# Kernel optimization log

Measured on AMD Instinct MI355X. Metric: run time of the kernel, lower is better.

## Reference

```python
import jax, jax.numpy as jnp
import numpy as np

GRID = 28
P = GRID * GRID  # 784 grid points
BY = 1.0 / 13.5  # grid spacing from DTMWeightWrapperLayer(by=1/13.5)
_c = BY * np.stack(np.meshgrid(np.arange(GRID), np.arange(GRID), indexing='ij'), -1).reshape(P, 2).astype(np.float32)
_D2np = ((_c[:, None, :] - _c[None, :, :]) ** 2).sum(-1)
_ORDERnp = np.argsort(_D2np, axis=1)  # per-grid-point neighbor order (constant)
D2S = jnp.asarray(np.take_along_axis(_D2np, _ORDERnp, axis=1), dtype=jnp.float32)  # [P,P] sorted sq dists
ORDER = jnp.asarray(_ORDERnp, dtype=jnp.int32)
TSEQ_A = jnp.asarray(np.linspace(0.06, 0.3, 25), dtype=jnp.float32); KK_A = (0, 1)
TSEQ_B = jnp.asarray(np.linspace(0.14, 0.4, 27), dtype=jnp.float32); KK_B = (0, 1, 2)

def _conv(x, k):
    return jax.lax.conv_general_dilated(x, k, (1, 1), 'SAME', dimension_numbers=('NHWC', 'HWIO', 'NHWC'))

def _dtm(w, m0):
    # distance-to-measure: w [B,P] nonneg weights on the 28x28 grid -> dtm values [B,P]
    ws = w[:, ORDER]                      # [B,P,P] weights ordered by distance from each grid point
    cum = jnp.cumsum(ws, axis=-1)
    m0W = m0 * jnp.sum(w, axis=-1)[:, None, None]  # mass threshold per sample
    eff = jnp.clip(m0W - (cum - ws), 0.0, ws)      # effective weight used from each neighbor
    return jnp.sqrt(jnp.sum(eff * D2S[None], axis=-1) / m0W[:, :, 0])

def _topo(f, tseq, kk, W, b):
    # persistence-landscape features: lambda_k(t) = k-th largest tent value over grid points
    tmax = tseq[-1]
    tent = jnp.maximum(0.0, jnp.minimum(tseq[None, :, None] - f[:, None, :], (tmax - tseq)[None, :, None]))  # [B,T,P]
    top, _ = jax.lax.top_k(tent, max(kk) + 1)       # [B,T,kmax]
    lam = top[..., jnp.asarray(kk)]                 # [B,T,|KK|]
    return lam.reshape(f.shape[0], -1) @ W + b

def setup_inputs() -> dict:
    key = jax.random.key(0)
    ks = jax.random.split(key, 16)
    r = lambda i, s: (0.05 * jax.random.normal(ks[i], s)).astype(jnp.float32)
    z = lambda n: jnp.zeros((n,), jnp.float32)
    return {
        'x': jax.random.uniform(ks[0], (16, 28, 28, 1), jnp.float32),
        'k11': r(1, (3, 3, 1, 32)), 'cb11': z(32), 'k12': r(2, (3, 3, 32, 1)), 'cb12': z(1),
        'k31': r(3, (3, 3, 1, 32)), 'cb31': z(32), 'k32': r(4, (3, 3, 32, 1)), 'cb32': z(1),
        'k41': r(5, (3, 3, 1, 32)), 'cb41': z(32), 'k42': r(6, (3, 3, 32, 1)), 'cb42': z(1),
        'W33': r(7, (50, 16)), 'b33': z(16), 'W43': r(8, (81, 16)), 'b43': z(16),
        'W5': r(9, (50, 16)), 'b5': z(16), 'W6': r(10, (81, 16)), 'b6': z(16),
        'W7': r(11, (848, 64)), 'b7': z(64), 'W8': r(12, (64, 10)), 'b8': z(10),
    }

def reference(x, k11, cb11, k12, cb12, k31, cb31, k32, cb32, k41, cb41, k42, cb42,
              W33, b33, W43, b43, W5, b5, W6, b6, W7, b7, W8, b8):
    relu = jax.nn.relu
    B = 16
    # CNN branch on raw image
    x1 = relu(_conv(relu(_conv(x, k11) + cb11), k12) + cb12).reshape(B, P)
    # DTM functions on the grid
    x2 = x.reshape(B, P)
    x2_1 = _dtm(x2, 0.05)
    x2_2 = _dtm(x2, 0.2)
    # CNN on DTM(m0=0.05) then topo layer
    x3 = relu(_conv(relu(_conv(x2_1.reshape(B, GRID, GRID, 1), k31) + cb31), k32) + cb32).reshape(B, P)
    x3 = relu(_topo(x3, TSEQ_A, KK_A, W33, b33))
    # CNN on DTM(m0=0.2) then topo layer
    x4 = relu(_conv(relu(_conv(x2_2.reshape(B, GRID, GRID, 1), k41) + cb41), k42) + cb42).reshape(B, P)
    x4 = relu(_topo(x4, TSEQ_B, KK_B, W43, b43))
    # topo layers directly on DTM functions
    x5 = relu(_topo(x2_1, TSEQ_A, KK_A, W5, b5))
    x6 = relu(_topo(x2_2, TSEQ_B, KK_B, W6, b6))
    xc = jnp.concatenate((x1, x3, x4, x5, x6), axis=-1)  # [16,848]
    return relu(xc @ W7 + b7) @ W8 + b8  # [16,10]
```

## Files before the change

kernel.cpp:

```cpp
#include <hip/hip_runtime.h>
#include <math.h>

#define GRID 28
#define NP 784
#define PADW 82
#define PADOFF 27

struct PairTab { unsigned int pk[NP]; float d2[NP]; };
constexpr PairTab make_pairs() {
    PairTab t{};
    int cnt[1459] = {};
    for (int di = 0; di < GRID; ++di)
        for (int dj = 0; dj < GRID; ++dj) cnt[di*di + dj*dj]++;
    int off[1459] = {};
    int acc = 0;
    for (int s = 0; s < 1459; ++s) { off[s] = acc; acc += cnt[s]; }
    const double BY2 = (1.0/13.5) * (1.0/13.5);
    for (int di = 0; di < GRID; ++di)
        for (int dj = 0; dj < GRID; ++dj) {
            int s = di*di + dj*dj;
            int o = off[s]++;
            t.pk[o] = (unsigned)(((di*PADW) << 6) | dj);
            t.d2[o] = (float)((double)s * BY2);
        }
    return t;
}
__constant__ PairTab d_PT = make_pairs();

__global__ __launch_bounds__(1024) void dtm_kernel(const float* __restrict__ x,
        float* __restrict__ ws)
{
    __shared__ float wpad[PADW*PADW];
    __shared__ float red[16];
    float* out1 = ws;
    float* out2 = ws + 12544;

    const int blk = blockIdx.x;
    const int img = blk / 49, grp = blk % 49;
    const int tid = threadIdx.x;
    const int w = tid >> 6, lane = tid & 63;

    for (int i = tid; i < PADW*PADW; i += 1024) wpad[i] = 0.f;
    float v = 0.f;
    if (tid < NP) v = x[img*NP + tid];
    __syncthreads();
    if (tid < NP) wpad[(tid/GRID + PADOFF)*PADW + (tid % GRID) + PADOFF] = v;
    for (int off = 32; off; off >>= 1) v += __shfl_down(v, off, 64);
    if (lane == 0) red[w] = v;
    __syncthreads();
    float sumw = 0.f;
    #pragma unroll
    for (int i = 0; i < 16; ++i) sumw += red[i];

    const int pix  = grp*16 + w;
    const int base = (pix/GRID + PADOFF)*PADW + (pix % GRID) + PADOFF;
    const float m0W1 = 0.05f * sumw;
    const float m0W2 = 0.2f  * sumw;
    float a1 = 0.f, a2 = 0.f, carry = 0.f;

    for (int k0 = 0; k0 < NP; k0 += 64) {
        const int idx = k0 + lane;
        const int ii  = idx < NP ? idx : NP-1;
        const unsigned p = d_PT.pk[ii];
        const float dd   = d_PT.d2[ii];
        const int a  = (int)(p >> 6);
        const int bb = (int)(p & 63u);
        const float w00 = wpad[base + a + bb];
        const float w01 = wpad[base + a - bb];
        const float w10 = wpad[base - a + bb];
        const float w11 = wpad[base - a - bb];
        float Wg = w00;
        Wg += (bb ? w01 : 0.f);
        Wg += (a  ? w10 : 0.f);
        Wg += ((a && bb) ? w11 : 0.f);
        if (idx >= NP) Wg = 0.f;
        float incl = Wg;
        #pragma unroll
        for (int d = 1; d < 64; d <<= 1) {
            const float t = __shfl_up(incl, d, 64);
            if (lane >= d) incl += t;
        }
        const float cumb = carry + (incl - Wg);
        const float e1 = fminf(fmaxf(m0W1 - cumb, 0.f), Wg);
        const float e2 = fminf(fmaxf(m0W2 - cumb, 0.f), Wg);
        a1 = fmaf(e1, dd, a1);
        a2 = fmaf(e2, dd, a2);
        carry += __shfl(incl, 63, 64);
        if (carry >= m0W2) break;
    }
    for (int m = 32; m; m >>= 1) { a1 += __shfl_xor(a1, m, 64); a2 += __shfl_xor(a2, m, 64); }
    if (lane == 0) {
        out1[img*NP + pix] = sqrtf(a1 / m0W1);
        out2[img*NP + pix] = sqrtf(a2 / m0W2);
    }
}

__device__ void conv_path_g(const float* __restrict__ inRow,
                            const float* __restrict__ kA, const float* __restrict__ cbA,
                            const float* __restrict__ kB, const float* __restrict__ cbB,
                            float* __restrict__ outRow, int r0, float* smem)
{
    float* inl = smem;
    float* kAl = inl + 308;
    float* cbl = kAl + 288;
    float* kBl = cbl + 32;
    float* h   = kBl + 288;
    const int tid = threadIdx.x;
    const float cbB0 = cbB[0];

    for (int i = tid; i < 288; i += 1024) { kAl[i] = kA[i]; kBl[i] = kB[i]; }
    if (tid < 32) cbl[tid] = cbA[tid];
    for (int i = tid; i < 11*GRID; i += 1024) {
        const int lr = i / GRID, xx = i % GRID;
        const int y = r0 - 2 + lr;
        inl[i] = (y >= 0 && y < GRID) ? inRow[y*GRID + xx] : 0.f;
    }
    __syncthreads();

    for (int o = tid; o < 9*GRID*32; o += 1024) {
        const int c = o & 31;
        const int pos = o >> 5;
        const int xx = pos % GRID;
        const int lr = pos / GRID;
        const int y = r0 - 1 + lr;
        if ((unsigned)y < GRID) {
            float a = cbl[c];
            #pragma unroll
            for (int dy = 0; dy < 3; ++dy) {
                const int iy = y + dy - 1;
                if ((unsigned)iy >= GRID) continue;
                const int il = iy - (r0 - 2);
                #pragma unroll
                for (int dx = 0; dx < 3; ++dx) {
                    const int ix = xx + dx - 1;
                    if ((unsigned)ix < GRID)
                        a = fmaf(inl[il*GRID + ix], kAl[(dy*3 + dx)*32 + c], a);
                }
            }
            h[(lr*GRID + xx)*33 + c] = fmaxf(a, 0.f);
        }
    }
    __syncthreads();

    if (tid < 4*7*GRID) {
        const int o = tid >> 2, part = tid & 3;
        const int xx = o % GRID, ly = o / GRID;
        const int y = r0 + ly;
        float a = 0.f;
        #pragma unroll
        for (int dy = 0; dy < 3; ++dy) {
            const int yy = y + dy - 1;
            if ((unsigned)yy >= GRID) continue;
            const int lr = yy - (r0 - 1);
            #pragma unroll
            for (int dx = 0; dx < 3; ++dx) {
                const int x2 = xx + dx - 1;
                if ((unsigned)x2 >= GRID) continue;
                const float* hb = &h[(lr*GRID + x2)*33 + part*8];
                const float* kb = &kBl[(dy*3 + dx)*32 + part*8];
                #pragma unroll
                for (int c = 0; c < 8; ++c) a += hb[c] * kb[c];
            }
        }
        a += __shfl_xor(a, 1, 64);
        a += __shfl_xor(a, 2, 64);
        if (part == 0) outRow[y*GRID + xx] = fmaxf(a + cbB0, 0.f);
    }
}

__global__ __launch_bounds__(1024) void conv_kernel(const float* __restrict__ x,
        const float* __restrict__ k11, const float* __restrict__ cb11,
        const float* __restrict__ k12, const float* __restrict__ cb12,
        const float* __restrict__ k31, const float* __restrict__ cb31,
        const float* __restrict__ k32, const float* __restrict__ cb32,
        const float* __restrict__ k41, const float* __restrict__ cb41,
        const float* __restrict__ k42, const float* __restrict__ cb42,
        float* __restrict__ ws)
{
    __shared__ float smem[9232];
    const int blk = blockIdx.x;
    const float* x2_1 = ws;
    const float* x2_2 = ws + 12544;
    float* x1o = ws + 25088;
    float* x3c = ws + 37632;
    float* x4c = ws + 50176;

    if (blk < 64) {
        const int b = blk >> 2, q = blk & 3;
        conv_path_g(x + b*NP, k11, cb11, k12, cb12, x1o + b*NP, q*7, smem);
    } else if (blk < 128) {
        const int cidx = blk - 64;
        const int b = cidx >> 2, q = cidx & 3;
        conv_path_g(x2_1 + b*NP, k31, cb31, k32, cb32, x3c + b*NP, q*7, smem);
    } else {
        const int cidx = blk - 128;
        const int b = cidx >> 2, q = cidx & 3;
        conv_path_g(x2_2 + b*NP, k41, cb41, k42, cb42, x4c + b*NP, q*7, smem);
    }
}

__device__ __forceinline__ float tseqA(int i) {
    if (i == 24) return 0.3f;
    return (float)((double)i * ((0.3 - 0.06)/24.0) + 0.06);
}
__device__ __forceinline__ float tseqB(int i) {
    if (i == 26) return 0.4f;
    return (float)((double)i * ((0.4 - 0.14)/26.0) + 0.14);
}

__device__ __forceinline__ void merge3(float& m0, float& m1, float& m2,
                                       float b0, float b1, float b2) {
    float r0, r1, r2;
    if (m0 <= b0) {
        r0 = m0;
        if (m1 <= b0) { r1 = m1; r2 = fminf(m2, b0); }
        else          { r1 = b0; r2 = fminf(m1, b1); }
    } else {
        r0 = b0;
        if (b1 <= m0) { r1 = b1; r2 = fminf(b2, m0); }
        else          { r1 = m0; r2 = fminf(m1, b1); }
    }
    m0 = r0; m1 = r1; m2 = r2;
}

__global__ __launch_bounds__(1024) void tail_kernel(
        const float* __restrict__ W33, const float* __restrict__ b33,
        const float* __restrict__ W43, const float* __restrict__ b43,
        const float* __restrict__ W5,  const float* __restrict__ b5,
        const float* __restrict__ W6,  const float* __restrict__ b6,
        const float* __restrict__ W7,  const float* __restrict__ b7,
        const float* __restrict__ W8,  const float* __restrict__ b8,
        const float* __restrict__ ws,  float* __restrict__ out)
{
    __shared__ float xc[848];
    __shared__ float part[1024];
    __shared__ float h7[64];
    __shared__ float fsh[16];
    const int b = blockIdx.x, tid = threadIdx.x;
    const int w = tid >> 6, lane = tid & 63;
    const float* x2_1 = ws;
    const float* x2_2 = ws + 12544;
    const float* x1o  = ws + 25088;
    const float* x3c  = ws + 37632;
    const float* x4c  = ws + 50176;

    if (tid < NP) xc[tid] = x1o[b*NP + tid];

    if (w < 4) {
        const float* src = (w == 0) ? x3c : (w == 1) ? x4c : (w == 2) ? x2_1 : x2_2;
        src += b*NP;
        float m0 = INFINITY, m1 = INFINITY, m2 = INFINITY;
        for (int i = lane; i < NP; i += 64) {
            const float v = src[i];
            if (v < m0)      { m2 = m1; m1 = m0; m0 = v; }
            else if (v < m1) { m2 = m1; m1 = v; }
            else if (v < m2) { m2 = v; }
        }
        for (int mask = 1; mask <= 32; mask <<= 1) {
            const float b0 = __shfl_xor(m0, mask, 64);
            const float b1 = __shfl_xor(m1, mask, 64);
            const float b2 = __shfl_xor(m2, mask, 64);
            merge3(m0, m1, m2, b0, b1, b2);
        }
        if (lane == 0) { fsh[w*3+0] = m0; fsh[w*3+1] = m1; fsh[w*3+2] = m2; }
    }
    __syncthreads();

    if (w < 4) {
        const int g = lane >> 4, j = lane & 15;
        const float f0 = fsh[w*3+0], f1 = fsh[w*3+1], f2 = fsh[w*3+2];
        float acc = 0.f;
        if (w == 0 || w == 2) {
            const float* Wm = (w == 0) ? W33 : W5;
            for (int i = g; i < 50; i += 4) {
                const int t = i >> 1, k = i & 1;
                const float ts = tseqA(t);
                const float fk = k ? f1 : f0;
                const float lam = fmaxf(fminf(ts - fk, 0.3f - ts), 0.f);
                acc = fmaf(lam, Wm[i*16 + j], acc);
            }
        } else {
            const float* Wm = (w == 1) ? W43 : W6;
            for (int i = g; i < 81; i += 4) {
                const int t = i / 3, k = i - t*3;
                const float ts = tseqB(t);
                const float fk = (k == 0) ? f0 : (k == 1 ? f1 : f2);
                const float lam = fmaxf(fminf(ts - fk, 0.4f - ts), 0.f);
                acc = fmaf(lam, Wm[i*16 + j], acc);
            }
        }
        acc += __shfl_xor(acc, 16, 64);
        acc += __shfl_xor(acc, 32, 64);
        if (lane < 16) {
            const float* bv = (w == 0) ? b33 : (w == 1) ? b43 : (w == 2) ? b5 : b6;
            xc[784 + w*16 + lane] = fmaxf(acc + bv[lane], 0.f);
        }
    }
    __syncthreads();

    {
        float acc = 0.f;
        const int i0 = w * 53;
        for (int i = i0; i < i0 + 53; ++i) acc = fmaf(xc[i], W7[i*64 + lane], acc);
        part[w*64 + lane] = acc;
    }
    __syncthreads();
    if (tid < 64) {
        float s = b7[tid];
        #pragma unroll
        for (int k = 0; k < 16; ++k) s += part[k*64 + tid];
        h7[tid] = fmaxf(s, 0.f);
    }
    __syncthreads();

    if (w < 10) {
        float a2 = h7[lane] * W8[lane*10 + w];
        for (int m = 32; m; m >>= 1) a2 += __shfl_down(a2, m, 64);
        if (lane == 0) out[b*10 + w] = a2 + b8[w];
    }
}

extern "C" void kernel_launch(void* const* d_in, const int* in_sizes, int n_in,
                              void* d_out, int out_size, void* d_ws, size_t ws_size,
                              hipStream_t stream)
{
    const float* x    = (const float*)d_in[0];
    const float* k11  = (const float*)d_in[1];
    const float* cb11 = (const float*)d_in[2];
    const float* k12  = (const float*)d_in[3];
    const float* cb12 = (const float*)d_in[4];
    const float* k31  = (const float*)d_in[5];
    const float* cb31 = (const float*)d_in[6];
    const float* k32  = (const float*)d_in[7];
    const float* cb32 = (const float*)d_in[8];
    const float* k41  = (const float*)d_in[9];
    const float* cb41 = (const float*)d_in[10];
    const float* k42  = (const float*)d_in[11];
    const float* cb42 = (const float*)d_in[12];
    const float* W33  = (const float*)d_in[13];
    const float* b33  = (const float*)d_in[14];
    const float* W43  = (const float*)d_in[15];
    const float* b43  = (const float*)d_in[16];
    const float* W5   = (const float*)d_in[17];
    const float* b5   = (const float*)d_in[18];
    const float* W6   = (const float*)d_in[19];
    const float* b6   = (const float*)d_in[20];
    const float* W7   = (const float*)d_in[21];
    const float* b7   = (const float*)d_in[22];
    const float* W8   = (const float*)d_in[23];
    const float* b8   = (const float*)d_in[24];
    float* ws  = (float*)d_ws;
    float* out = (float*)d_out;

    dtm_kernel <<<dim3(784), dim3(1024), 0, stream>>>(x, ws);
    conv_kernel<<<dim3(192), dim3(1024), 0, stream>>>(x, k11, cb11, k12, cb12,
                                                      k31, cb31, k32, cb32,
                                                      k41, cb41, k42, cb42, ws);
    tail_kernel<<<dim3(16),  dim3(1024), 0, stream>>>(W33, b33, W43, b43, W5, b5, W6, b6,
                                                      W7, b7, W8, b8, ws, out);
}
```

Measured before the change: 35.43 us.

## Fuse conv and tail kernels via last-block atomic counter; drop padded DTM smem

Merges the conv and tail kernels into one launch. Each image's 12 conv blocks bump a per-image atomic counter, and the last block to arrive runs the topo/MLP tail for that image. The counter is zeroed by block 0 of the preceding DTM kernel. Separately, the DTM kernel replaces the 82x82 zero-padded shared buffer with an unpadded 784-float image plus explicit bounds checks, which removes the zero-fill and a barrier. The cost is extra branch and predicate work in the DTM inner loop and a reliance on atomics plus fences for correctness.

```diff
diff --git a/kernel.cpp b/kernel.cpp
--- a/kernel.cpp
+++ b/kernel.cpp
@@ -3,8 +3,6 @@
 
 #define GRID 28
 #define NP 784
-#define PADW 82
-#define PADOFF 27
 
 struct PairTab { unsigned int pk[NP]; float d2[NP]; };
 constexpr PairTab make_pairs() {
@@ -20,7 +18,7 @@
         for (int dj = 0; dj < GRID; ++dj) {
             int s = di*di + dj*dj;
             int o = off[s]++;
-            t.pk[o] = (unsigned)(((di*PADW) << 6) | dj);
+            t.pk[o] = (unsigned)((di << 8) | dj);
             t.d2[o] = (float)((double)s * BY2);
         }
     return t;
@@ -30,7 +28,7 @@
 __global__ __launch_bounds__(1024) void dtm_kernel(const float* __restrict__ x,
         float* __restrict__ ws)
 {
-    __shared__ float wpad[PADW*PADW];
+    __shared__ float wimg[NP];
     __shared__ float red[16];
     float* out1 = ws;
     float* out2 = ws + 12544;
@@ -40,11 +38,10 @@
     const int tid = threadIdx.x;
     const int w = tid >> 6, lane = tid & 63;
 
-    for (int i = tid; i < PADW*PADW; i += 1024) wpad[i] = 0.f;
+    if (blk == 0 && tid < 16) ((int*)(ws + 62720))[tid] = 0;
+
     float v = 0.f;
-    if (tid < NP) v = x[img*NP + tid];
-    __syncthreads();
-    if (tid < NP) wpad[(tid/GRID + PADOFF)*PADW + (tid % GRID) + PADOFF] = v;
+    if (tid < NP) { v = x[img*NP + tid]; wimg[tid] = v; }
     for (int off = 32; off; off >>= 1) v += __shfl_down(v, off, 64);
     if (lane == 0) red[w] = v;
     __syncthreads();
@@ -52,8 +49,8 @@
     #pragma unroll
     for (int i = 0; i < 16; ++i) sumw += red[i];
 
-    const int pix  = grp*16 + w;
-    const int base = (pix/GRID + PADOFF)*PADW + (pix % GRID) + PADOFF;
+    const int pix = grp*16 + w;
+    const int pr = pix / GRID, pc = pix % GRID;
     const float m0W1 = 0.05f * sumw;
     const float m0W2 = 0.2f  * sumw;
     float a1 = 0.f, a2 = 0.f, carry = 0.f;
@@ -63,16 +60,18 @@
         const int ii  = idx < NP ? idx : NP-1;
         const unsigned p = d_PT.pk[ii];
         const float dd   = d_PT.d2[ii];
-        const int a  = (int)(p >> 6);
-        const int bb = (int)(p & 63u);
-        const float w00 = wpad[base + a + bb];
-        const float w01 = wpad[base + a - bb];
-        const float w10 = wpad[base - a + bb];
-        const float w11 = wpad[base - a - bb];
-        float Wg = w00;
-        Wg += (bb ? w01 : 0.f);
-        Wg += (a  ? w10 : 0.f);
-        Wg += ((a && bb) ? w11 : 0.f);
+        const int di = (int)(p >> 8);
+        const int dj = (int)(p & 255u);
+        const int dG = di * GRID;
+        const bool rpOK = (pr + di) < GRID;
+        const bool rmOK = pr >= di;
+        const bool cpOK = (pc + dj) < GRID;
+        const bool cmOK = pc >= dj;
+        float Wg = 0.f;
+        if (rpOK && cpOK)               Wg += wimg[pix + dG + dj];
+        if (dj && rpOK && cmOK)         Wg += wimg[pix + dG - dj];
+        if (di && rmOK && cpOK)         Wg += wimg[pix - dG + dj];
+        if (di && dj && rmOK && cmOK)   Wg += wimg[pix - dG - dj];
         if (idx >= NP) Wg = 0.f;
         float incl = Wg;
         #pragma unroll
@@ -168,37 +167,6 @@
     }
 }
 
-__global__ __launch_bounds__(1024) void conv_kernel(const float* __restrict__ x,
-        const float* __restrict__ k11, const float* __restrict__ cb11,
-        const float* __restrict__ k12, const float* __restrict__ cb12,
-        const float* __restrict__ k31, const float* __restrict__ cb31,
-        const float* __restrict__ k32, const float* __restrict__ cb32,
-        const float* __restrict__ k41, const float* __restrict__ cb41,
-        const float* __restrict__ k42, const float* __restrict__ cb42,
-        float* __restrict__ ws)
-{
-    __shared__ float smem[9232];
-    const int blk = blockIdx.x;
-    const float* x2_1 = ws;
-    const float* x2_2 = ws + 12544;
-    float* x1o = ws + 25088;
-    float* x3c = ws + 37632;
-    float* x4c = ws + 50176;
-
-    if (blk < 64) {
-        const int b = blk >> 2, q = blk & 3;
-        conv_path_g(x + b*NP, k11, cb11, k12, cb12, x1o + b*NP, q*7, smem);
-    } else if (blk < 128) {
-        const int cidx = blk - 64;
-        const int b = cidx >> 2, q = cidx & 3;
-        conv_path_g(x2_1 + b*NP, k31, cb31, k32, cb32, x3c + b*NP, q*7, smem);
-    } else {
-        const int cidx = blk - 128;
-        const int b = cidx >> 2, q = cidx & 3;
-        conv_path_g(x2_2 + b*NP, k41, cb41, k42, cb42, x4c + b*NP, q*7, smem);
-    }
-}
-
 __device__ __forceinline__ float tseqA(int i) {
     if (i == 24) return 0.3f;
     return (float)((double)i * ((0.3 - 0.06)/24.0) + 0.06);
@@ -223,26 +191,58 @@
     m0 = r0; m1 = r1; m2 = r2;
 }
 
-__global__ __launch_bounds__(1024) void tail_kernel(
+__global__ __launch_bounds__(1024) void conv_tail_kernel(const float* __restrict__ x,
+        const float* __restrict__ k11, const float* __restrict__ cb11,
+        const float* __restrict__ k12, const float* __restrict__ cb12,
+        const float* __restrict__ k31, const float* __restrict__ cb31,
+        const float* __restrict__ k32, const float* __restrict__ cb32,
+        const float* __restrict__ k41, const float* __restrict__ cb41,
+        const float* __restrict__ k42, const float* __restrict__ cb42,
         const float* __restrict__ W33, const float* __restrict__ b33,
         const float* __restrict__ W43, const float* __restrict__ b43,
         const float* __restrict__ W5,  const float* __restrict__ b5,
         const float* __restrict__ W6,  const float* __restrict__ b6,
         const float* __restrict__ W7,  const float* __restrict__ b7,
         const float* __restrict__ W8,  const float* __restrict__ b8,
-        const float* __restrict__ ws,  float* __restrict__ out)
+        float* __restrict__ ws, float* __restrict__ out)
 {
-    __shared__ float xc[848];
-    __shared__ float part[1024];
-    __shared__ float h7[64];
-    __shared__ float fsh[16];
-    const int b = blockIdx.x, tid = threadIdx.x;
-    const int w = tid >> 6, lane = tid & 63;
+    __shared__ float smem[9232];
+    __shared__ int lastFlag;
+    const int blk = blockIdx.x;
+    const int tid = threadIdx.x;
     const float* x2_1 = ws;
     const float* x2_2 = ws + 12544;
-    const float* x1o  = ws + 25088;
-    const float* x3c  = ws + 37632;
-    const float* x4c  = ws + 50176;
+    float* x1o = ws + 25088;
+    float* x3c = ws + 37632;
+    float* x4c = ws + 50176;
+    int* cnt = (int*)(ws + 62720);
+
+    int b;
+    if (blk < 64) {
+        b = blk >> 2;
+        conv_path_g(x + b*NP, k11, cb11, k12, cb12, x1o + b*NP, (blk & 3)*7, smem);
+    } else if (blk < 128) {
+        const int c = blk - 64; b = c >> 2;
+        conv_path_g(x2_1 + b*NP, k31, cb31, k32, cb32, x3c + b*NP, (c & 3)*7, smem);
+    } else {
+        const int c = blk - 128; b = c >> 2;
+        conv_path_g(x2_2 + b*NP, k41, cb41, k42, cb42, x4c + b*NP, (c & 3)*7, smem);
+    }
+
+    __threadfence();
+    __syncthreads();
+    if (tid == 0)
+        lastFlag = (__hip_atomic_fetch_add(&cnt[b], 1, __ATOMIC_ACQ_REL,
+                                           __HIP_MEMORY_SCOPE_AGENT) == 11);
+    __syncthreads();
+    if (!lastFlag) return;
+    __threadfence();
+
+    float* xc   = smem;
+    float* part = smem + 848;
+    float* h7   = smem + 1872;
+    float* fsh  = smem + 1936;
+    const int w = tid >> 6, lane = tid & 63;
 
     if (tid < NP) xc[tid] = x1o[b*NP + tid];
 
@@ -352,10 +352,11 @@
     float* ws  = (float*)d_ws;
     float* out = (float*)d_out;
 
-    dtm_kernel <<<dim3(784), dim3(1024), 0, stream>>>(x, ws);
-    conv_kernel<<<dim3(192), dim3(1024), 0, stream>>>(x, k11, cb11, k12, cb12,
-                                                      k31, cb31, k32, cb32,
-                                                      k41, cb41, k42, cb42, ws);
-    tail_kernel<<<dim3(16),  dim3(1024), 0, stream>>>(W33, b33, W43, b43, W5, b5, W6, b6,
-                                                      W7, b7, W8, b8, ws, out);
-}
+    dtm_kernel      <<<dim3(784), dim3(1024), 0, stream>>>(x, ws);
+    conv_tail_kernel<<<dim3(192), dim3(1024), 0, stream>>>(x, k11, cb11, k12, cb12,
+                                                           k31, cb31, k32, cb32,
+                                                           k41, cb41, k42, cb42,
+                                                           W33, b33, W43, b43, W5, b5,
+                                                           W6, b6, W7, b7, W8, b8,
+                                                           ws, out);
+}
```

After: 96.61 us. +172.7%, slower.

## Move raw-image conv into DTM launch and split convs into smaller row bands

Applied to the files above, without the earlier changes.

The raw-image CNN branch, which does not depend on the DTM, now runs inside the first launch alongside the DTM blocks, leaving the second launch with only the two DTM-dependent conv paths. Convolutions are split into 7 bands of 4 rows instead of 4 bands of 7, so the grid has more and smaller blocks with less halo recompute per block. The DTM no longer builds a zero-padded 82x82 shared image; it reads the unpadded 28x28 image with explicit bounds checks, which drops the clear loop and one barrier. The price is extra branch logic in the inner neighbor loop and less shared memory per block.

```diff
diff --git a/kernel.cpp b/kernel.cpp
--- a/kernel.cpp
+++ b/kernel.cpp
@@ -3,8 +3,6 @@
 
 #define GRID 28
 #define NP 784
-#define PADW 82
-#define PADOFF 27
 
 struct PairTab { unsigned int pk[NP]; float d2[NP]; };
 constexpr PairTab make_pairs() {
@@ -20,104 +18,37 @@
         for (int dj = 0; dj < GRID; ++dj) {
             int s = di*di + dj*dj;
             int o = off[s]++;
-            t.pk[o] = (unsigned)(((di*PADW) << 6) | dj);
+            t.pk[o] = (unsigned)((di << 8) | dj);
             t.d2[o] = (float)((double)s * BY2);
         }
     return t;
 }
 __constant__ PairTab d_PT = make_pairs();
 
-__global__ __launch_bounds__(1024) void dtm_kernel(const float* __restrict__ x,
-        float* __restrict__ ws)
-{
-    __shared__ float wpad[PADW*PADW];
-    __shared__ float red[16];
-    float* out1 = ws;
-    float* out2 = ws + 12544;
-
-    const int blk = blockIdx.x;
-    const int img = blk / 49, grp = blk % 49;
-    const int tid = threadIdx.x;
-    const int w = tid >> 6, lane = tid & 63;
-
-    for (int i = tid; i < PADW*PADW; i += 1024) wpad[i] = 0.f;
-    float v = 0.f;
-    if (tid < NP) v = x[img*NP + tid];
-    __syncthreads();
-    if (tid < NP) wpad[(tid/GRID + PADOFF)*PADW + (tid % GRID) + PADOFF] = v;
-    for (int off = 32; off; off >>= 1) v += __shfl_down(v, off, 64);
-    if (lane == 0) red[w] = v;
-    __syncthreads();
-    float sumw = 0.f;
-    #pragma unroll
-    for (int i = 0; i < 16; ++i) sumw += red[i];
-
-    const int pix  = grp*16 + w;
-    const int base = (pix/GRID + PADOFF)*PADW + (pix % GRID) + PADOFF;
-    const float m0W1 = 0.05f * sumw;
-    const float m0W2 = 0.2f  * sumw;
-    float a1 = 0.f, a2 = 0.f, carry = 0.f;
-
-    for (int k0 = 0; k0 < NP; k0 += 64) {
-        const int idx = k0 + lane;
-        const int ii  = idx < NP ? idx : NP-1;
-        const unsigned p = d_PT.pk[ii];
-        const float dd   = d_PT.d2[ii];
-        const int a  = (int)(p >> 6);
-        const int bb = (int)(p & 63u);
-        const float w00 = wpad[base + a + bb];
-        const float w01 = wpad[base + a - bb];
-        const float w10 = wpad[base - a + bb];
-        const float w11 = wpad[base - a - bb];
-        float Wg = w00;
-        Wg += (bb ? w01 : 0.f);
-        Wg += (a  ? w10 : 0.f);
-        Wg += ((a && bb) ? w11 : 0.f);
-        if (idx >= NP) Wg = 0.f;
-        float incl = Wg;
-        #pragma unroll
-        for (int d = 1; d < 64; d <<= 1) {
-            const float t = __shfl_up(incl, d, 64);
-            if (lane >= d) incl += t;
-        }
-        const float cumb = carry + (incl - Wg);
-        const float e1 = fminf(fmaxf(m0W1 - cumb, 0.f), Wg);
-        const float e2 = fminf(fmaxf(m0W2 - cumb, 0.f), Wg);
-        a1 = fmaf(e1, dd, a1);
-        a2 = fmaf(e2, dd, a2);
-        carry += __shfl(incl, 63, 64);
-        if (carry >= m0W2) break;
-    }
-    for (int m = 32; m; m >>= 1) { a1 += __shfl_xor(a1, m, 64); a2 += __shfl_xor(a2, m, 64); }
-    if (lane == 0) {
-        out1[img*NP + pix] = sqrtf(a1 / m0W1);
-        out2[img*NP + pix] = sqrtf(a2 / m0W2);
-    }
-}
-
-__device__ void conv_path_g(const float* __restrict__ inRow,
-                            const float* __restrict__ kA, const float* __restrict__ cbA,
-                            const float* __restrict__ kB, const float* __restrict__ cbB,
-                            float* __restrict__ outRow, int r0, float* smem)
+__device__ void conv_band(const float* __restrict__ in,
+                          const float* __restrict__ kA, const float* __restrict__ cbA,
+                          const float* __restrict__ kB, const float* __restrict__ cbB,
+                          float* __restrict__ outImg, int r0, float* smem)
 {
     float* inl = smem;
-    float* kAl = inl + 308;
-    float* cbl = kAl + 288;
-    float* kBl = cbl + 32;
-    float* h   = kBl + 288;
+    float* kAl = inl + 224;
+    float* kBl = kAl + 288;
+    float* cbl = kBl + 288;
+    float* h   = cbl + 32;
     const int tid = threadIdx.x;
     const float cbB0 = cbB[0];
 
-    for (int i = tid; i < 288; i += 1024) { kAl[i] = kA[i]; kBl[i] = kB[i]; }
-    if (tid < 32) cbl[tid] = cbA[tid];
-    for (int i = tid; i < 11*GRID; i += 1024) {
+    if (tid < 288) { kAl[tid] = kA[tid]; kBl[tid] = kB[tid]; }
+    else if (tid < 320) cbl[tid - 288] = cbA[tid - 288];
+    else if (tid < 320 + 8*GRID) {
+        const int i = tid - 320;
         const int lr = i / GRID, xx = i % GRID;
         const int y = r0 - 2 + lr;
-        inl[i] = (y >= 0 && y < GRID) ? inRow[y*GRID + xx] : 0.f;
-    }
-    __syncthreads();
-
-    for (int o = tid; o < 9*GRID*32; o += 1024) {
+        inl[i] = ((unsigned)y < GRID) ? in[y*GRID + xx] : 0.f;
+    }
+    __syncthreads();
+
+    for (int o = tid; o < 6*GRID*32; o += 1024) {
         const int c = o & 31;
         const int pos = o >> 5;
         const int xx = pos % GRID;
@@ -142,7 +73,7 @@
     }
     __syncthreads();
 
-    if (tid < 4*7*GRID) {
+    if (tid < 4*4*GRID) {
         const int o = tid >> 2, part = tid & 3;
         const int xx = o % GRID, ly = o / GRID;
         const int y = r0 + ly;
@@ -164,38 +95,108 @@
         }
         a += __shfl_xor(a, 1, 64);
         a += __shfl_xor(a, 2, 64);
-        if (part == 0) outRow[y*GRID + xx] = fmaxf(a + cbB0, 0.f);
-    }
-}
-
-__global__ __launch_bounds__(1024) void conv_kernel(const float* __restrict__ x,
+        if (part == 0) outImg[y*GRID + xx] = fmaxf(a + cbB0, 0.f);
+    }
+}
+
+__global__ __launch_bounds__(1024) void k1_kernel(const float* __restrict__ x,
         const float* __restrict__ k11, const float* __restrict__ cb11,
         const float* __restrict__ k12, const float* __restrict__ cb12,
+        float* __restrict__ ws)
+{
+    __shared__ float smem[6376];
+    const int blk = blockIdx.x;
+    const int tid = threadIdx.x;
+
+    if (blk < 112) {
+        const int img = blk / 7, band = blk % 7;
+        conv_band(x + img*NP, k11, cb11, k12, cb12, ws + 25088 + img*NP, band*4, smem);
+        return;
+    }
+
+    float* wimg = smem;
+    float* red  = smem + 784;
+    float* out1 = ws;
+    float* out2 = ws + 12544;
+    const int dblk = blk - 112;
+    const int img = dblk / 49, grp = dblk % 49;
+    const int w = tid >> 6, lane = tid & 63;
+
+    float v = 0.f;
+    if (tid < NP) { v = x[img*NP + tid]; wimg[tid] = v; }
+    for (int off = 32; off; off >>= 1) v += __shfl_down(v, off, 64);
+    if (lane == 0) red[w] = v;
+    __syncthreads();
+    float sumw = 0.f;
+    #pragma unroll
+    for (int i = 0; i < 16; ++i) sumw += red[i];
+
+    const int pix = grp*16 + w;
+    const int pr = pix / GRID, pc = pix % GRID;
+    const float m0W1 = 0.05f * sumw;
+    const float m0W2 = 0.2f  * sumw;
+    float a1 = 0.f, a2 = 0.f, carry = 0.f;
+
+    for (int k0 = 0; k0 < NP; k0 += 64) {
+        const int idx = k0 + lane;
+        const int ii  = idx < NP ? idx : NP-1;
+        const unsigned p = d_PT.pk[ii];
+        const float dd   = d_PT.d2[ii];
+        const int di = (int)(p >> 8);
+        const int dj = (int)(p & 255u);
+        const int dG = di * GRID;
+        const bool rpOK = (pr + di) < GRID;
+        const bool rmOK = pr >= di;
+        const bool cpOK = (pc + dj) < GRID;
+        const bool cmOK = pc >= dj;
+        float Wg = 0.f;
+        if (rpOK && cpOK)               Wg += wimg[pix + dG + dj];
+        if (dj && rpOK && cmOK)         Wg += wimg[pix + dG - dj];
+        if (di && rmOK && cpOK)         Wg += wimg[pix - dG + dj];
+        if (di && dj && rmOK && cmOK)   Wg += wimg[pix - dG - dj];
+        if (idx >= NP) Wg = 0.f;
+        float incl = Wg;
+        #pragma unroll
+        for (int d = 1; d < 64; d <<= 1) {
+            const float t = __shfl_up(incl, d, 64);
+            if (lane >= d) incl += t;
+        }
+        const float cumb = carry + (incl - Wg);
+        const float e1 = fminf(fmaxf(m0W1 - cumb, 0.f), Wg);
+        const float e2 = fminf(fmaxf(m0W2 - cumb, 0.f), Wg);
+        a1 = fmaf(e1, dd, a1);
+        a2 = fmaf(e2, dd, a2);
+        carry += __shfl(incl, 63, 64);
+        if (carry >= m0W2) break;
+    }
+    for (int m = 32; m; m >>= 1) { a1 += __shfl_xor(a1, m, 64); a2 += __shfl_xor(a2, m, 64); }
+    if (lane == 0) {
+        out1[img*NP + pix] = sqrtf(a1 / m0W1);
+        out2[img*NP + pix] = sqrtf(a2 / m0W2);
+    }
+}
+
+__global__ __launch_bounds__(1024) void k2_kernel(
         const float* __restrict__ k31, const float* __restrict__ cb31,
         const float* __restrict__ k32, const float* __restrict__ cb32,
         const float* __restrict__ k41, const float* __restrict__ cb41,
         const float* __restrict__ k42, const float* __restrict__ cb42,
         float* __restrict__ ws)
 {
-    __shared__ float smem[9232];
+    __shared__ float smem[6376];
     const int blk = blockIdx.x;
     const float* x2_1 = ws;
     const float* x2_2 = ws + 12544;
-    float* x1o = ws + 25088;
     float* x3c = ws + 37632;
     float* x4c = ws + 50176;
 
-    if (blk < 64) {
-        const int b = blk >> 2, q = blk & 3;
-        conv_path_g(x + b*NP, k11, cb11, k12, cb12, x1o + b*NP, q*7, smem);
-    } else if (blk < 128) {
-        const int cidx = blk - 64;
-        const int b = cidx >> 2, q = cidx & 3;
-        conv_path_g(x2_1 + b*NP, k31, cb31, k32, cb32, x3c + b*NP, q*7, smem);
+    if (blk < 112) {
+        const int img = blk / 7, band = blk % 7;
+        conv_band(x2_1 + img*NP, k31, cb31, k32, cb32, x3c + img*NP, band*4, smem);
     } else {
-        const int cidx = blk - 128;
-        const int b = cidx >> 2, q = cidx & 3;
-        conv_path_g(x2_2 + b*NP, k41, cb41, k42, cb42, x4c + b*NP, q*7, smem);
+        const int c = blk - 112;
+        const int img = c / 7, band = c % 7;
+        conv_band(x2_2 + img*NP, k41, cb41, k42, cb42, x4c + img*NP, band*4, smem);
     }
 }
 
@@ -352,9 +353,8 @@
     float* ws  = (float*)d_ws;
     float* out = (float*)d_out;
 
-    dtm_kernel <<<dim3(784), dim3(1024), 0, stream>>>(x, ws);
-    conv_kernel<<<dim3(192), dim3(1024), 0, stream>>>(x, k11, cb11, k12, cb12,
-                                                      k31, cb31, k32, cb32,
+    k1_kernel  <<<dim3(896), dim3(1024), 0, stream>>>(x, k11, cb11, k12, cb12, ws);
+    k2_kernel  <<<dim3(224), dim3(1024), 0, stream>>>(k31, cb31, k32, cb32,
                                                       k41, cb41, k42, cb42, ws);
     tail_kernel<<<dim3(16),  dim3(1024), 0, stream>>>(W33, b33, W43, b43, W5, b5, W6, b6,
                                                       W7, b7, W8, b8, ws, out);
```

Result: faster. 32.62 us (-7.9%).
